# Performance work log

Hardware: AMD Instinct MI355X
Metric: run time of the kernel (lower is better)

The kernel has to match this reference:

```python
import jax, jax.numpy as jnp
import numpy as np

N, E = 100000, 1600000
IN, HID, HEADS, OUT = 128, 16, 4, 64
SLOPE = 0.2  # leaky_relu negative_slope default


def setup_inputs() -> dict:
    key = jax.random.key(0)
    ks = jax.random.split(key, 12)
    s = 0.1  # xavier-ish scale
    return {
        "x": jax.random.normal(ks[0], (N, IN), jnp.float32),
        "edge_index": jax.random.randint(ks[1], (2, E), 0, N, jnp.int32),
        "W1": jax.random.normal(ks[2], (IN, HEADS * HID), jnp.float32) * s,
        "att_l1": jax.random.normal(ks[3], (1, HEADS, HID), jnp.float32) * s,
        "att_r1": jax.random.normal(ks[4], (1, HEADS, HID), jnp.float32) * s,
        "res_W1": jax.random.normal(ks[5], (IN, HEADS * HID), jnp.float32) * s,
        "b1": jnp.zeros((HEADS * HID,), jnp.float32),
        "W2": jax.random.normal(ks[6], (HEADS * HID, OUT), jnp.float32) * s,
        "att_l2": jax.random.normal(ks[7], (1, 1, OUT), jnp.float32) * s,
        "att_r2": jax.random.normal(ks[8], (1, 1, OUT), jnp.float32) * s,
        "b2": jnp.zeros((OUT,), jnp.float32),
    }


def agdn_conv(x, W, att_l, att_r, bias, res_W, src, dst):
    # x: [n, in]; W: [in, H*C]; att_*: [1, H, C]
    n = x.shape[0]
    H, C = att_l.shape[1], att_l.shape[2]
    x_lin = (x @ W).reshape(n, H, C)
    # residual: res_fc if present, else identity on x_lin (residual=True path)
    x_res = (x @ res_W) if res_W is not None else x_lin.reshape(n, H * C)
    al = jnp.sum(x_lin * att_l, axis=-1)  # [n, H]
    ar = jnp.sum(x_lin * att_r, axis=-1)  # [n, H]
    logits = jax.nn.leaky_relu(al[src] + ar[dst], SLOPE)  # [E, H]
    # segment softmax over incoming edges of each dst node
    m = jax.ops.segment_max(logits, dst, num_segments=n)
    e = jnp.exp(logits - m[dst])
    ssum = jax.ops.segment_sum(e, dst, num_segments=n)
    alpha = e / (ssum[dst] + 1e-16)  # [E, H]
    msg = x_lin[src] * alpha[:, :, None]  # [E, H, C]
    out = jax.ops.segment_sum(msg, dst, num_segments=n).reshape(n, H * C)
    return out + x_res + bias


def reference(x, edge_index, W1, att_l1, att_r1, res_W1, b1, W2, att_l2, att_r2, b2):
    src, dst = edge_index[0], edge_index[1]
    h = agdn_conv(x, W1, att_l1, att_r1, b1, res_W1, src, dst)
    h = jax.nn.elu(h)
    # last layer: heads=1, in==heads*out so res_fc is None (residual = x_lin)
    return agdn_conv(h, W2, att_l2, att_r2, b2, None, src, dst)
```

## Files before the change

kernel.cpp:

```cpp
#include <hip/hip_runtime.h>
#include <hip/hip_bf16.h>
#include <hip/hip_fp16.h>
#include <math.h>

#define NN 100000
#define EE 1600000
#define IN_DIM 128
#define HID 16
#define HEADS 4
#define D1 64
#define OUT_DIM 64
#define SLOPE 0.2f

#define NB 391
#define BCAP 5120
#define BINA_CHUNK 4096
#define BINA_BLOCKS ((EE + BINA_CHUNK - 1) / BINA_CHUNK)
#define NODE_BLOCKS ((NN + 63) / 64)
#define AGG_BLOCKS (NN / 32)

#define W1COLS 144
#define LDB1 272
#define LDB2 144

typedef __attribute__((ext_vector_type(8))) short bf16x8;
typedef __attribute__((ext_vector_type(4))) float f32x4;

__device__ __forceinline__ float leaky(float v) { return v > 0.f ? v : SLOPE * v; }
__device__ __forceinline__ unsigned short f2bf(float f) {
    __hip_bfloat16 h = __float2bfloat16(f);
    return *(unsigned short*)&h;
}
__device__ __forceinline__ __half2 u2h2(unsigned u) {
    union { unsigned u; __half2 h; } c; c.u = u; return c.h;
}
__device__ __forceinline__ bf16x8 pack8(float4 a, float4 b) {
    bf16x8 r;
    r[0] = (short)f2bf(a.x); r[1] = (short)f2bf(a.y);
    r[2] = (short)f2bf(a.z); r[3] = (short)f2bf(a.w);
    r[4] = (short)f2bf(b.x); r[5] = (short)f2bf(b.y);
    r[6] = (short)f2bf(b.z); r[7] = (short)f2bf(b.w);
    return r;
}

__global__ void prep_kernel(int* __restrict__ bucket_cursor,
                            const float* __restrict__ W1,
                            const float* __restrict__ resW,
                            const float* __restrict__ W2,
                            const float* __restrict__ attl1,
                            const float* __restrict__ attr1,
                            const float* __restrict__ attl2,
                            const float* __restrict__ attr2,
                            unsigned short* __restrict__ Wtb,
                            unsigned short* __restrict__ W2tb,
                            float* __restrict__ vl, float* __restrict__ vr) {
    int t = threadIdx.x;
    if (blockIdx.x == 0) {
        if (t < NB) bucket_cursor[t] = t * BCAP;
    } else if (blockIdx.x == 1) {
        for (int idx = t; idx < W1COLS * 128; idx += 512) {
            int col = idx >> 7, k = idx & 127;
            float w = 0.f;
            if (col < 64) {
                w = W1[k * 64 + col];
            } else if (col < 128) {
                w = resW[k * 64 + (col - 64)];
            } else if (col < 132) {
                int hh = col - 128;
                for (int c = 0; c < HID; c++)
                    w += W1[k * 64 + hh * HID + c] * attl1[hh * HID + c];
            } else if (col < 136) {
                int hh = col - 132;
                for (int c = 0; c < HID; c++)
                    w += W1[k * 64 + hh * HID + c] * attr1[hh * HID + c];
            }
            Wtb[idx] = f2bf(w);
        }
    } else {
        for (int idx = t; idx < 64 * 64; idx += 512) {
            int col = idx >> 6, k = idx & 63;
            W2tb[idx] = f2bf(W2[k * 64 + col]);
        }
        if (t < D1) {
            float a = 0.f, b = 0.f;
            for (int o = 0; o < OUT_DIM; o++) {
                float w = W2[t * OUT_DIM + o];
                a += w * attl2[o];
                b += w * attr2[o];
            }
            vl[t] = a; vr[t] = b;
        }
    }
}

__device__ __forceinline__ void binA_body(char* smem, int bid,
        const int* __restrict__ src, const int* __restrict__ dst,
        int* __restrict__ bucket_cursor, unsigned* __restrict__ binned) {
    unsigned* spack = (unsigned*)smem;
    unsigned short* sbkt = (unsigned short*)(smem + 16384);
    int* lhist = (int*)(smem + 24576);
    int* lscan = lhist + 512;
    int* gbase = lscan + 512;
    int* lcur  = gbase + 512;
    int* wtot  = (int*)(smem + 32768);
    int t = threadIdx.x;
    lhist[t] = 0; lhist[t + 256] = 0;
    lcur[t] = 0;  lcur[t + 256] = 0;
    __syncthreads();
    int e0 = bid * BINA_CHUNK;
    int nvalid = EE - e0; if (nvalid > BINA_CHUNK) nvalid = BINA_CHUNK;
    unsigned pk[16];
    unsigned short bk[16];
#pragma unroll
    for (int i = 0; i < 16; i++) {
        int e = e0 + t + i * 256;
        if (e < EE) {
            int d = dst[e], s = src[e];
            int b = d >> 8;
            pk[i] = ((unsigned)(d & 255) << 24) | (unsigned)s;
            bk[i] = (unsigned short)b;
            atomicAdd(&lhist[b], 1);
        } else bk[i] = 0xFFFFu;
    }
    __syncthreads();
    int a = lhist[2 * t], b = lhist[2 * t + 1];
    int ps = a + b;
    int lane = t & 63, wv = t >> 6;
    int inc = ps;
#pragma unroll
    for (int off = 1; off < 64; off <<= 1) {
        int n = __shfl_up(inc, off, 64);
        if (lane >= off) inc += n;
    }
    if (lane == 63) wtot[wv] = inc;
    __syncthreads();
    int wbase = 0;
#pragma unroll
    for (int i = 0; i < 4; i++) if (i < wv) wbase += wtot[i];
    int excl = wbase + inc - ps;
    lscan[2 * t] = excl;
    lscan[2 * t + 1] = excl + a;
    if (a) gbase[2 * t] = atomicAdd(&bucket_cursor[2 * t], a);
    if (b) gbase[2 * t + 1] = atomicAdd(&bucket_cursor[2 * t + 1], b);
    __syncthreads();
#pragma unroll
    for (int i = 0; i < 16; i++) {
        if (bk[i] != 0xFFFFu) {
            int bb = bk[i];
            int pos = atomicAdd(&lcur[bb], 1);
            int slot = lscan[bb] + pos;
            spack[slot] = pk[i];
            sbkt[slot] = (unsigned short)bb;
        }
    }
    __syncthreads();
    for (int j = t; j < nvalid; j += 256) {
        int bb = sbkt[j];
        int idx = gbase[bb] + (j - lscan[bb]);
        if (idx < (bb + 1) * BCAP) binned[idx] = spack[j];
    }
}

__device__ __forceinline__ void node1_body(char* smemB, int bid,
        const float* __restrict__ x, const unsigned short* __restrict__ Wtb,
        const float* __restrict__ b1, __half* __restrict__ xlin1h,
        __half* __restrict__ acc1h, float* __restrict__ al1,
        float* __restrict__ ar1) {
    int t = threadIdx.x;
    int base = bid * 64;
    int wave = t >> 6, lane = t & 63;
    int quad = lane >> 4, li = lane & 15;
    int node = base + wave * 16 + li;

    uint4 breg[9];
#pragma unroll
    for (int s = 0; s < 9; s++) {
        int seg = s * 256 + t;
        breg[s] = *(const uint4*)(Wtb + (seg >> 4) * 128 + (seg & 15) * 8);
    }
    float4 xreg[8];
#pragma unroll
    for (int i = 0; i < 8; i++) xreg[i] = make_float4(0.f, 0.f, 0.f, 0.f);
    if (node < NN) {
        const float* xp = x + (size_t)node * IN_DIM + quad * 8;
#pragma unroll
        for (int kc = 0; kc < 4; kc++) {
            xreg[kc * 2]     = *(const float4*)(xp + kc * 32);
            xreg[kc * 2 + 1] = *(const float4*)(xp + kc * 32 + 4);
        }
    }
#pragma unroll
    for (int s = 0; s < 9; s++) {
        int seg = s * 256 + t;
        *(uint4*)(smemB + (seg >> 4) * LDB1 + (seg & 15) * 16) = breg[s];
    }
    __syncthreads();

    f32x4 accs[9];
#pragma unroll
    for (int nt = 0; nt < 9; nt++) accs[nt] = (f32x4){0.f, 0.f, 0.f, 0.f};
#pragma unroll
    for (int kc = 0; kc < 4; kc++) {
        bf16x8 afrag = pack8(xreg[kc * 2], xreg[kc * 2 + 1]);
        const char* brow = smemB + kc * 64 + quad * 16;
#pragma unroll
        for (int nt = 0; nt < 9; nt++) {
            bf16x8 bfrag = *(const bf16x8*)(brow + (nt * 16 + li) * LDB1);
            accs[nt] = __builtin_amdgcn_mfma_f32_16x16x32_bf16(afrag, bfrag, accs[nt], 0, 0, 0);
        }
    }

    int m0 = base + wave * 16;
#pragma unroll
    for (int nt = 0; nt < 4; nt++) {
#pragma unroll
        for (int j = 0; j < 4; j++) {
            int nd = m0 + quad * 4 + j;
            if (nd < NN) xlin1h[(size_t)nd * D1 + nt * 16 + li] = __float2half(accs[nt][j]);
        }
    }
#pragma unroll
    for (int nt = 4; nt < 8; nt++) {
        int col = (nt - 4) * 16 + li;
        float bv = b1[col];
#pragma unroll
        for (int j = 0; j < 4; j++) {
            int nd = m0 + quad * 4 + j;
            if (nd < NN) acc1h[(size_t)nd * D1 + col] = __float2half(accs[nt][j] + bv);
        }
    }
#pragma unroll
    for (int j = 0; j < 4; j++) {
        int nd = m0 + quad * 4 + j;
        if (nd < NN) {
            if (li < 4) al1[nd * HEADS + li] = accs[8][j];
            else if (li < 8) ar1[nd * HEADS + (li - 4)] = accs[8][j];
        }
    }
}

__global__ __launch_bounds__(256, 4) void fusedA_kernel(
        const int* __restrict__ src, const int* __restrict__ dst,
        int* __restrict__ bucket_cursor, unsigned* __restrict__ binned,
        const float* __restrict__ x, const unsigned short* __restrict__ Wtb,
        const float* __restrict__ b1, __half* __restrict__ xlin1h,
        __half* __restrict__ acc1h, float* __restrict__ al1,
        float* __restrict__ ar1) {
    __shared__ __align__(16) char smem[W1COLS * LDB1];
    if (blockIdx.x < BINA_BLOCKS)
        binA_body(smem, blockIdx.x, src, dst, bucket_cursor, binned);
    else
        node1_body(smem, blockIdx.x - BINA_BLOCKS, x, Wtb, b1, xlin1h, acc1h, al1, ar1);
}

__global__ __launch_bounds__(256) void binB_kernel(const unsigned* __restrict__ binned,
                                                   const int* __restrict__ bucket_cursor,
                                                   int* __restrict__ row_ptr,
                                                   int* __restrict__ counts,
                                                   int* __restrict__ sorted_src) {
    __shared__ int lcount[256], lrow[256], lcur[256];
    __shared__ int wtot[4];
    int b = blockIdx.x, t = threadIdx.x;
    int start = b * BCAP;
    int cnt = bucket_cursor[b] - start;
    if (cnt > BCAP) cnt = BCAP;
    lcount[t] = 0;
    __syncthreads();
    for (int i = t; i < cnt; i += 256) {
        atomicAdd(&lcount[binned[start + i] >> 24], 1);
    }
    __syncthreads();
    int v = lcount[t];
    int lane = t & 63, wv = t >> 6;
    int inc = v;
#pragma unroll
    for (int off = 1; off < 64; off <<= 1) {
        int n = __shfl_up(inc, off, 64);
        if (lane >= off) inc += n;
    }
    if (lane == 63) wtot[wv] = inc;
    __syncthreads();
    int wbase = 0;
#pragma unroll
    for (int i = 0; i < 4; i++) if (i < wv) wbase += wtot[i];
    int ex = wbase + inc - v;
    lrow[t] = ex;
    lcur[t] = 0;
    int node = (b << 8) + t;
    if (node < NN) {
        row_ptr[node] = start + ex;
        counts[node] = v;
    }
    __syncthreads();
    for (int i = t; i < cnt; i += 256) {
        unsigned p = binned[start + i];
        int low = p >> 24;
        int pos = atomicAdd(&lcur[low], 1);
        sorted_src[start + lrow[low] + pos] = (int)(p & 0xFFFFFFu);
    }
}

__global__ __launch_bounds__(256) void agg1_kernel(
        const int* __restrict__ sorted_src, const int* __restrict__ row_ptr,
        const int* __restrict__ counts,
        const float* __restrict__ al1, const float* __restrict__ ar1,
        const __half* __restrict__ xlin1h, const __half* __restrict__ acc1h,
        __half* __restrict__ hh,
        const float* __restrict__ vl, const float* __restrict__ vr,
        float* __restrict__ al2, float* __restrict__ ar2) {
    __shared__ __half s_alpha[4][8][65][4];
    int w = threadIdx.x >> 6, lane = threadIdx.x & 63;
    int g = lane >> 3, li = lane & 7;
    int d = blockIdx.x * 32 + w * 8 + g;
    int rs = row_ptr[d];
    int deg = counts[d];
    const float4 arv = *(const float4*)(ar1 + d * 4);
    int h = li >> 1;

    int maxdeg = deg;
    maxdeg = max(maxdeg, __shfl_xor(maxdeg, 8, 64));
    maxdeg = max(maxdeg, __shfl_xor(maxdeg, 16, 64));
    maxdeg = max(maxdeg, __shfl_xor(maxdeg, 32, 64));
    bool big = maxdeg > 64;

    float s0 = 0.f, s1 = 0.f, s2 = 0.f, s3 = 0.f;
    if (!big) {
#pragma unroll
        for (int it = 0; it < 8; it++) {
            int e = li + it * 8;
            if (e < deg) {
                int s = sorted_src[rs + e];
                const float4 alv = *(const float4*)(al1 + s * 4);
                float e0 = __expf(leaky(alv.x + arv.x));
                float e1 = __expf(leaky(alv.y + arv.y));
                float e2 = __expf(leaky(alv.z + arv.z));
                float e3 = __expf(leaky(alv.w + arv.w));
                s0 += e0; s1 += e1; s2 += e2; s3 += e3;
                __half2 h01 = __floats2half2_rn(e0, e1);
                __half2 h23 = __floats2half2_rn(e2, e3);
                *(uint2*)&s_alpha[w][g][e][0] =
                    make_uint2(*(unsigned*)&h01, *(unsigned*)&h23);
            }
        }
    } else {
        for (int e = li; e < deg; e += 8) {
            int s = sorted_src[rs + e];
            const float4 alv = *(const float4*)(al1 + s * 4);
            s0 += __expf(leaky(alv.x + arv.x));
            s1 += __expf(leaky(alv.y + arv.y));
            s2 += __expf(leaky(alv.z + arv.z));
            s3 += __expf(leaky(alv.w + arv.w));
        }
    }
#pragma unroll
    for (int off = 1; off < 8; off <<= 1) {
        s0 += __shfl_xor(s0, off, 64);
        s1 += __shfl_xor(s1, off, 64);
        s2 += __shfl_xor(s2, off, 64);
        s3 += __shfl_xor(s3, off, 64);
    }
    float inv0 = 0.f, inv1 = 0.f, inv2 = 0.f, inv3 = 0.f;
    if (deg > 0) {
        inv0 = 1.f / (s0 + 1e-16f); inv1 = 1.f / (s1 + 1e-16f);
        inv2 = 1.f / (s2 + 1e-16f); inv3 = 1.f / (s3 + 1e-16f);
    }
    float invh = (h == 0) ? inv0 : (h == 1) ? inv1 : (h == 2) ? inv2 : inv3;
    __half2 invh2 = __floats2half2_rn(invh, invh);

    __half2 a01 = __floats2half2_rn(0.f, 0.f);
    __half2 a23 = a01, a45 = a01, a67 = a01;
    float fb0=0.f, fb1=0.f, fb2=0.f, fb3=0.f, fb4=0.f, fb5=0.f, fb6=0.f, fb7=0.f;
    if (!big) {
        for (int i0 = 0; i0 < maxdeg; i0 += 8) {
            int myi = i0 + li;
            int mys = (myi < deg) ? sorted_src[rs + myi] : 0;
            int ss[8]; __half ah[8]; uint4 uu[8];
#pragma unroll
            for (int j = 0; j < 8; j++) {
                ss[j] = __shfl(mys, (g << 3) + j, 64);
                int i = i0 + j;
                ah[j] = (i < deg) ? s_alpha[w][g][i][h] : __float2half(0.f);
            }
#pragma unroll
            for (int j = 0; j < 8; j++) {
                int i = i0 + j;
                uu[j] = make_uint4(0u, 0u, 0u, 0u);
                if (i < deg) uu[j] = *(const uint4*)(xlin1h + (size_t)ss[j] * D1 + li * 8);
            }
#pragma unroll
            for (int j = 0; j < 8; j++) {
                __half2 a2 = __hmul2(__half2half2(ah[j]), invh2);
                a01 = __hfma2(a2, u2h2(uu[j].x), a01);
                a23 = __hfma2(a2, u2h2(uu[j].y), a23);
                a45 = __hfma2(a2, u2h2(uu[j].z), a45);
                a67 = __hfma2(a2, u2h2(uu[j].w), a67);
            }
        }
    } else {
        float arh = (h == 0) ? arv.x : (h == 1) ? arv.y : (h == 2) ? arv.z : arv.w;
        for (int i = 0; i < deg; i++) {
            int s = sorted_src[rs + i];
            const float4 alv = *(const float4*)(al1 + s * 4);
            float lv = (h == 0) ? alv.x : (h == 1) ? alv.y : (h == 2) ? alv.z : alv.w;
            float a = __expf(leaky(lv + arh)) * invh;
            uint4 u = *(const uint4*)(xlin1h + (size_t)s * D1 + li * 8);
            float2 x01 = __half22float2(u2h2(u.x));
            float2 x23 = __half22float2(u2h2(u.y));
            float2 x45 = __half22float2(u2h2(u.z));
            float2 x67 = __half22float2(u2h2(u.w));
            fb0 += a * x01.x; fb1 += a * x01.y; fb2 += a * x23.x; fb3 += a * x23.y;
            fb4 += a * x45.x; fb5 += a * x45.y; fb6 += a * x67.x; fb7 += a * x67.y;
        }
    }
    float c0, c1, c2, c3, c4, c5, c6, c7;
    { float2 tv;
      tv = __half22float2(a01); c0 = tv.x + fb0; c1 = tv.y + fb1;
      tv = __half22float2(a23); c2 = tv.x + fb2; c3 = tv.y + fb3;
      tv = __half22float2(a45); c4 = tv.x + fb4; c5 = tv.y + fb5;
      tv = __half22float2(a67); c6 = tv.x + fb6; c7 = tv.y + fb7; }
    uint4 rres = *(const uint4*)(acc1h + (size_t)d * D1 + li * 8);
    { float2 tv;
      tv = __half22float2(u2h2(rres.x)); c0 += tv.x; c1 += tv.y;
      tv = __half22float2(u2h2(rres.y)); c2 += tv.x; c3 += tv.y;
      tv = __half22float2(u2h2(rres.z)); c4 += tv.x; c5 += tv.y;
      tv = __half22float2(u2h2(rres.w)); c6 += tv.x; c7 += tv.y; }
    c0 = c0 > 0.f ? c0 : (__expf(c0) - 1.f);
    c1 = c1 > 0.f ? c1 : (__expf(c1) - 1.f);
    c2 = c2 > 0.f ? c2 : (__expf(c2) - 1.f);
    c3 = c3 > 0.f ? c3 : (__expf(c3) - 1.f);
    c4 = c4 > 0.f ? c4 : (__expf(c4) - 1.f);
    c5 = c5 > 0.f ? c5 : (__expf(c5) - 1.f);
    c6 = c6 > 0.f ? c6 : (__expf(c6) - 1.f);
    c7 = c7 > 0.f ? c7 : (__expf(c7) - 1.f);
    __half2 o01 = __floats2half2_rn(c0, c1);
    __half2 o23 = __floats2half2_rn(c2, c3);
    __half2 o45 = __floats2half2_rn(c4, c5);
    __half2 o67 = __floats2half2_rn(c6, c7);
    uint4 hv = make_uint4(*(unsigned*)&o01, *(unsigned*)&o23,
                          *(unsigned*)&o45, *(unsigned*)&o67);
    *(uint4*)(hh + (size_t)d * D1 + li * 8) = hv;
    const float4 vla = *(const float4*)(vl + li * 8);
    const float4 vlb = *(const float4*)(vl + li * 8 + 4);
    const float4 vra = *(const float4*)(vr + li * 8);
    const float4 vrb = *(const float4*)(vr + li * 8 + 4);
    float pl = c0 * vla.x + c1 * vla.y + c2 * vla.z + c3 * vla.w
             + c4 * vlb.x + c5 * vlb.y + c6 * vlb.z + c7 * vlb.w;
    float pr = c0 * vra.x + c1 * vra.y + c2 * vra.z + c3 * vra.w
             + c4 * vrb.x + c5 * vrb.y + c6 * vrb.z + c7 * vrb.w;
#pragma unroll
    for (int off = 1; off < 8; off <<= 1) {
        pl += __shfl_xor(pl, off, 64);
        pr += __shfl_xor(pr, off, 64);
    }
    if (li == 0) { al2[d] = pl; ar2[d] = pr; }
}

__global__ __launch_bounds__(256) void agg2_kernel(
        const int* __restrict__ sorted_src, const int* __restrict__ row_ptr,
        const int* __restrict__ counts,
        const float* __restrict__ al2, const float* __restrict__ ar2,
        const __half* __restrict__ hh,
        unsigned short* __restrict__ hsum) {
    __shared__ __half s_alpha[4][8][65];
    __shared__ int    s_src[4][8][65];
    int w = threadIdx.x >> 6, lane = threadIdx.x & 63;
    int g = lane >> 3, li = lane & 7;
    int d = blockIdx.x * 32 + w * 8 + g;
    int rs = row_ptr[d];
    int deg = counts[d];
    float ard = ar2[d];

    int maxdeg = deg;
    maxdeg = max(maxdeg, __shfl_xor(maxdeg, 8, 64));
    maxdeg = max(maxdeg, __shfl_xor(maxdeg, 16, 64));
    maxdeg = max(maxdeg, __shfl_xor(maxdeg, 32, 64));
    bool big = maxdeg > 64;

    float ssum = 0.f;
    if (!big) {
#pragma unroll
        for (int it = 0; it < 8; it++) {
            int e = li + it * 8;
            if (e < deg) {
                int s = sorted_src[rs + e];
                float ex = __expf(leaky(al2[s] + ard));
                ssum += ex;
                s_alpha[w][g][e] = __float2half(ex);
                s_src[w][g][e] = s;
            }
        }
    } else {
        for (int e = li; e < deg; e += 8) {
            int s = sorted_src[rs + e];
            ssum += __expf(leaky(al2[s] + ard));
        }
    }
#pragma unroll
    for (int off = 1; off < 8; off <<= 1) ssum += __shfl_xor(ssum, off, 64);
    float inv = (deg > 0) ? 1.f / (ssum + 1e-16f) : 0.f;
    __half2 inv2h = __floats2half2_rn(inv, inv);

    __half2 a01 = __floats2half2_rn(0.f, 0.f);
    __half2 a23 = a01, a45 = a01, a67 = a01;
    float fb0=0.f, fb1=0.f, fb2=0.f, fb3=0.f, fb4=0.f, fb5=0.f, fb6=0.f, fb7=0.f;
    if (!big) {
        for (int i0 = 0; i0 < maxdeg; i0 += 8) {
            int ss[8]; __half ah[8]; uint4 uu[8];
#pragma unroll
            for (int j = 0; j < 8; j++) {
                int i = i0 + j;
                bool v = i < deg;
                ss[j] = v ? s_src[w][g][i] : 0;
                ah[j] = v ? s_alpha[w][g][i] : __float2half(0.f);
            }
#pragma unroll
            for (int j = 0; j < 8; j++) {
                int i = i0 + j;
                uu[j] = make_uint4(0u, 0u, 0u, 0u);
                if (i < deg) uu[j] = *(const uint4*)(hh + (size_t)ss[j] * D1 + li * 8);
            }
#pragma unroll
            for (int j = 0; j < 8; j++) {
                __half2 a2 = __hmul2(__half2half2(ah[j]), inv2h);
                a01 = __hfma2(a2, u2h2(uu[j].x), a01);
                a23 = __hfma2(a2, u2h2(uu[j].y), a23);
                a45 = __hfma2(a2, u2h2(uu[j].z), a45);
                a67 = __hfma2(a2, u2h2(uu[j].w), a67);
            }
        }
    } else {
        for (int i = 0; i < deg; i++) {
            int s = sorted_src[rs + i];
            float a = __expf(leaky(al2[s] + ard)) * inv;
            uint4 u = *(const uint4*)(hh + (size_t)s * D1 + li * 8);
            float2 x01 = __half22float2(u2h2(u.x));
            float2 x23 = __half22float2(u2h2(u.y));
            float2 x45 = __half22float2(u2h2(u.z));
            float2 x67 = __half22float2(u2h2(u.w));
            fb0 += a * x01.x; fb1 += a * x01.y; fb2 += a * x23.x; fb3 += a * x23.y;
            fb4 += a * x45.x; fb5 += a * x45.y; fb6 += a * x67.x; fb7 += a * x67.y;
        }
    }
    float c0, c1, c2, c3, c4, c5, c6, c7;
    { float2 tv;
      tv = __half22float2(a01); c0 = tv.x + fb0; c1 = tv.y + fb1;
      tv = __half22float2(a23); c2 = tv.x + fb2; c3 = tv.y + fb3;
      tv = __half22float2(a45); c4 = tv.x + fb4; c5 = tv.y + fb5;
      tv = __half22float2(a67); c6 = tv.x + fb6; c7 = tv.y + fb7; }
    uint4 own = *(const uint4*)(hh + (size_t)d * D1 + li * 8);
    { float2 tv;
      tv = __half22float2(u2h2(own.x)); c0 += tv.x; c1 += tv.y;
      tv = __half22float2(u2h2(own.y)); c2 += tv.x; c3 += tv.y;
      tv = __half22float2(u2h2(own.z)); c4 += tv.x; c5 += tv.y;
      tv = __half22float2(u2h2(own.w)); c6 += tv.x; c7 += tv.y; }
    union { unsigned short us[8]; uint4 u4; } hw;
    hw.us[0] = f2bf(c0); hw.us[1] = f2bf(c1); hw.us[2] = f2bf(c2); hw.us[3] = f2bf(c3);
    hw.us[4] = f2bf(c4); hw.us[5] = f2bf(c5); hw.us[6] = f2bf(c6); hw.us[7] = f2bf(c7);
    *(uint4*)(hsum + (size_t)d * D1 + li * 8) = hw.u4;
}

__global__ __launch_bounds__(256) void node3_kernel(
        const unsigned short* __restrict__ hsum,
        const unsigned short* __restrict__ W2tb,
        const float* __restrict__ b2,
        float* __restrict__ out) {
    __shared__ char smemB[64 * LDB2];
    int t = threadIdx.x;
    int base = blockIdx.x * 64;
    int wave = t >> 6, lane = t & 63;
    int quad = lane >> 4, li = lane & 15;
    int node = base + wave * 16 + li;

    uint4 breg[2];
#pragma unroll
    for (int s = 0; s < 2; s++) {
        int seg = s * 256 + t;
        breg[s] = *(const uint4*)(W2tb + (seg >> 3) * 64 + (seg & 7) * 8);
    }
    bf16x8 afr[2];
#pragma unroll
    for (int kc = 0; kc < 2; kc++)
#pragma unroll
        for (int i = 0; i < 8; i++) afr[kc][i] = 0;
    if (node < NN) {
        afr[0] = *(const bf16x8*)(hsum + (size_t)node * D1 + quad * 8);
        afr[1] = *(const bf16x8*)(hsum + (size_t)node * D1 + 32 + quad * 8);
    }
#pragma unroll
    for (int s = 0; s < 2; s++) {
        int seg = s * 256 + t;
        *(uint4*)(smemB + (seg >> 3) * LDB2 + (seg & 7) * 16) = breg[s];
    }
    __syncthreads();

    f32x4 accs[4];
#pragma unroll
    for (int nt = 0; nt < 4; nt++) accs[nt] = (f32x4){0.f, 0.f, 0.f, 0.f};
#pragma unroll
    for (int kc = 0; kc < 2; kc++) {
        const char* brow = smemB + kc * 64 + quad * 16;
#pragma unroll
        for (int nt = 0; nt < 4; nt++) {
            bf16x8 bfrag = *(const bf16x8*)(brow + (nt * 16 + li) * LDB2);
            accs[nt] = __builtin_amdgcn_mfma_f32_16x16x32_bf16(afr[kc], bfrag, accs[nt], 0, 0, 0);
        }
    }

    int m0 = base + wave * 16;
#pragma unroll
    for (int nt = 0; nt < 4; nt++) {
        int col = nt * 16 + li;
        float bv = b2[col];
#pragma unroll
        for (int j = 0; j < 4; j++) {
            int nd = m0 + quad * 4 + j;
            if (nd < NN) out[(size_t)nd * OUT_DIM + col] = accs[nt][j] + bv;
        }
    }
}

extern "C" void kernel_launch(void* const* d_in, const int* in_sizes, int n_in,
                              void* d_out, int out_size, void* d_ws, size_t ws_size,
                              hipStream_t stream) {
    const float* x     = (const float*)d_in[0];
    const int*   eidx  = (const int*)d_in[1];
    const float* W1    = (const float*)d_in[2];
    const float* attl1 = (const float*)d_in[3];
    const float* attr1 = (const float*)d_in[4];
    const float* resW1 = (const float*)d_in[5];
    const float* b1    = (const float*)d_in[6];
    const float* W2    = (const float*)d_in[7];
    const float* attl2 = (const float*)d_in[8];
    const float* attr2 = (const float*)d_in[9];
    const float* b2    = (const float*)d_in[10];

    const int* src = eidx;
    const int* dst = eidx + EE;

    __half* xlin1h = (__half*)d_ws;
    __half* acc1h  = xlin1h + (size_t)NN * D1;
    __half* hh     = acc1h + (size_t)NN * D1;
    unsigned short* hsum = (unsigned short*)(hh + (size_t)NN * D1);
    float* al1   = (float*)(hsum + (size_t)NN * D1);
    float* ar1   = al1 + (size_t)NN * HEADS;
    float* al2   = ar1 + (size_t)NN * HEADS;
    float* ar2   = al2 + NN;
    float* vl    = ar2 + NN;
    float* vr    = vl + D1;
    unsigned short* Wtb  = (unsigned short*)(vr + D1);
    unsigned short* W2tb = Wtb + W1COLS * 128;
    int* counts        = (int*)(W2tb + 64 * 64);
    int* row_ptr       = counts + NN;
    int* bucket_cursor = row_ptr + NN;
    int* sorted_src    = bucket_cursor + 512;
    unsigned* binned = (unsigned*)d_out;

    float* out = (float*)d_out;

    prep_kernel<<<3, 512, 0, stream>>>(bucket_cursor, W1, resW1, W2,
                                       attl1, attr1, attl2, attr2,
                                       Wtb, W2tb, vl, vr);
    fusedA_kernel<<<BINA_BLOCKS + NODE_BLOCKS, 256, 0, stream>>>(
        src, dst, bucket_cursor, binned,
        x, Wtb, b1, xlin1h, acc1h, al1, ar1);
    binB_kernel<<<NB, 256, 0, stream>>>(binned, bucket_cursor,
                                        row_ptr, counts, sorted_src);

    agg1_kernel<<<AGG_BLOCKS, 256, 0, stream>>>(sorted_src, row_ptr, counts,
                                                al1, ar1, xlin1h, acc1h, hh,
                                                vl, vr, al2, ar2);

    agg2_kernel<<<AGG_BLOCKS, 256, 0, stream>>>(sorted_src, row_ptr, counts,
                                                al2, ar2, hh, hsum);
    node3_kernel<<<NODE_BLOCKS, 256, 0, stream>>>(hsum, W2tb, b2, out);
}
```

Measured before the change: 250.1 us.

## Scatter binned edges directly and stage node1 outputs in LDS for vector stores

The binning step no longer builds a local prefix scan and an LDS-sorted staging buffer. Each edge now claims a global slot through the per-bucket cursor and is written straight to the binned array, which drops a scan, a barrier and an LDS round trip but makes the global writes less coalesced. Separately, node1 results (xlin1 and acc1 in fp16) are first gathered into shared memory and then written out with 16-byte vector stores instead of scattered 2-byte stores. This adds an extra barrier and reuses the B-matrix LDS region after the MFMA loop.

```diff
diff --git a/kernel.cpp b/kernel.cpp
--- a/kernel.cpp
+++ b/kernel.cpp
@@ -96,19 +96,14 @@
 __device__ __forceinline__ void binA_body(char* smem, int bid,
         const int* __restrict__ src, const int* __restrict__ dst,
         int* __restrict__ bucket_cursor, unsigned* __restrict__ binned) {
-    unsigned* spack = (unsigned*)smem;
-    unsigned short* sbkt = (unsigned short*)(smem + 16384);
-    int* lhist = (int*)(smem + 24576);
-    int* lscan = lhist + 512;
-    int* gbase = lscan + 512;
-    int* lcur  = gbase + 512;
-    int* wtot  = (int*)(smem + 32768);
+    int* lhist = (int*)smem;
+    int* lcur  = lhist + 512;
+    int* gbase = lcur + 512;
     int t = threadIdx.x;
     lhist[t] = 0; lhist[t + 256] = 0;
     lcur[t] = 0;  lcur[t + 256] = 0;
     __syncthreads();
     int e0 = bid * BINA_CHUNK;
-    int nvalid = EE - e0; if (nvalid > BINA_CHUNK) nvalid = BINA_CHUNK;
     unsigned pk[16];
     unsigned short bk[16];
 #pragma unroll
@@ -123,41 +118,18 @@
         } else bk[i] = 0xFFFFu;
     }
     __syncthreads();
-    int a = lhist[2 * t], b = lhist[2 * t + 1];
-    int ps = a + b;
-    int lane = t & 63, wv = t >> 6;
-    int inc = ps;
-#pragma unroll
-    for (int off = 1; off < 64; off <<= 1) {
-        int n = __shfl_up(inc, off, 64);
-        if (lane >= off) inc += n;
-    }
-    if (lane == 63) wtot[wv] = inc;
-    __syncthreads();
-    int wbase = 0;
-#pragma unroll
-    for (int i = 0; i < 4; i++) if (i < wv) wbase += wtot[i];
-    int excl = wbase + inc - ps;
-    lscan[2 * t] = excl;
-    lscan[2 * t + 1] = excl + a;
-    if (a) gbase[2 * t] = atomicAdd(&bucket_cursor[2 * t], a);
-    if (b) gbase[2 * t + 1] = atomicAdd(&bucket_cursor[2 * t + 1], b);
+    int c1 = lhist[t], c2 = lhist[t + 256];
+    if (c1) gbase[t] = atomicAdd(&bucket_cursor[t], c1);
+    if (c2) gbase[t + 256] = atomicAdd(&bucket_cursor[t + 256], c2);
     __syncthreads();
 #pragma unroll
     for (int i = 0; i < 16; i++) {
         if (bk[i] != 0xFFFFu) {
-            int bb = bk[i];
-            int pos = atomicAdd(&lcur[bb], 1);
-            int slot = lscan[bb] + pos;
-            spack[slot] = pk[i];
-            sbkt[slot] = (unsigned short)bb;
-        }
-    }
-    __syncthreads();
-    for (int j = t; j < nvalid; j += 256) {
-        int bb = sbkt[j];
-        int idx = gbase[bb] + (j - lscan[bb]);
-        if (idx < (bb + 1) * BCAP) binned[idx] = spack[j];
+            int b = bk[i];
+            int pos = atomicAdd(&lcur[b], 1);
+            int idx = gbase[b] + pos;
+            if (idx < (b + 1) * BCAP) binned[idx] = pk[i];
+        }
     }
 }
 
@@ -210,13 +182,15 @@
         }
     }
 
-    int m0 = base + wave * 16;
+    __syncthreads();
+    __half* sx = (__half*)smemB;
+    __half* sa = sx + 64 * 64;
 #pragma unroll
     for (int nt = 0; nt < 4; nt++) {
 #pragma unroll
         for (int j = 0; j < 4; j++) {
-            int nd = m0 + quad * 4 + j;
-            if (nd < NN) xlin1h[(size_t)nd * D1 + nt * 16 + li] = __float2half(accs[nt][j]);
+            int rl = wave * 16 + quad * 4 + j;
+            sx[rl * 64 + nt * 16 + li] = __float2half(accs[nt][j]);
         }
     }
 #pragma unroll
@@ -225,10 +199,22 @@
         float bv = b1[col];
 #pragma unroll
         for (int j = 0; j < 4; j++) {
-            int nd = m0 + quad * 4 + j;
-            if (nd < NN) acc1h[(size_t)nd * D1 + col] = __float2half(accs[nt][j] + bv);
-        }
-    }
+            int rl = wave * 16 + quad * 4 + j;
+            sa[rl * 64 + col] = __float2half(accs[nt][j] + bv);
+        }
+    }
+    __syncthreads();
+    for (int i = t; i < 512; i += 256) {
+        int row = i >> 3, seg = i & 7;
+        int nd = base + row;
+        if (nd < NN) {
+            *(uint4*)(xlin1h + (size_t)nd * D1 + seg * 8) =
+                *(const uint4*)(sx + row * 64 + seg * 8);
+            *(uint4*)(acc1h + (size_t)nd * D1 + seg * 8) =
+                *(const uint4*)(sa + row * 64 + seg * 8);
+        }
+    }
+    int m0 = base + wave * 16;
 #pragma unroll
     for (int j = 0; j < 4; j++) {
         int nd = m0 + quad * 4 + j;
```

New measurement: 243.2 us. 1.03x faster.
